# Kernel optimization log

Measured on AMD Instinct MI355X. Metric: run time of the kernel, lower is better.

The kernel has to match this reference:

```python
import jax, jax.numpy as jnp
import numpy as np

N, E = 50000, 800000
IN_CH, HID, OUT_CH = 128, 256, 40
L, R = 3, 16
EPS = 1e-12


def setup_inputs() -> dict:
    key = jax.random.key(0)
    ks = jax.random.split(key, 16)
    s = 0.05
    return {
        'x': jax.random.normal(ks[0], (N, IN_CH), jnp.float32),
        'edge_index': jax.random.randint(ks[1], (2, E), 0, N, dtype=jnp.int64),
        'W_in': jax.random.normal(ks[2], (IN_CH, HID), jnp.float32) * s,
        'b_in': jnp.zeros((HID,), jnp.float32),
        'centers': jax.random.normal(ks[3], (L, R, HID), jnp.float32),
        'log_sigma': jnp.zeros((L, R, HID), jnp.float32),
        'W_rule': jax.random.normal(ks[4], (L, R, HID, HID), jnp.float32) * s,
        'b_rule': jnp.zeros((L, R, HID), jnp.float32),
        'W_self': jax.random.normal(ks[5], (L, HID, HID), jnp.float32) * s,
        'b_self': jnp.zeros((L, HID), jnp.float32),
        'gamma': jnp.ones((L, HID), jnp.float32),
        'beta': jnp.zeros((L, HID), jnp.float32),
        'W_h1': jax.random.normal(ks[6], (HID, HID // 2), jnp.float32) * s,
        'b_h1': jnp.zeros((HID // 2,), jnp.float32),
        'W_h2': jax.random.normal(ks[7], (HID // 2, OUT_CH), jnp.float32) * s,
        'b_h2': jnp.zeros((OUT_CH,), jnp.float32),
    }


def membership(h, c, log_s):
    # Gaussian rule firing, expanded to matmuls to avoid [N,R,H] distance tensor
    inv_s2 = jnp.exp(-2.0 * log_s)                         # [R,H]
    d = (h * h) @ inv_s2.T - 2.0 * (h @ (c * inv_s2).T) \
        + jnp.sum(c * c * inv_s2, axis=-1)                 # [N,R]
    firing = jnp.exp(-0.5 * d)
    return firing / (jnp.sum(firing, axis=-1, keepdims=True) + EPS)


def fmpl(h, src, dst, c, log_s, W_r, b_r, W_s, b_s):
    n = h.shape[0]
    deg = jax.ops.segment_sum(jnp.ones(src.shape[0], h.dtype), dst, num_segments=n)
    agg = jax.ops.segment_sum(h[src], dst, num_segments=n) / jnp.clip(deg, 1.0)[:, None]
    mu = membership(h, c, log_s)                           # [N,R]
    per_rule = jnp.einsum('ni,rio->nro', agg, W_r) + b_r[None]  # [N,R,H]
    fuzzy = jnp.einsum('nr,nro->no', mu, per_rule)
    return h @ W_s + b_s + fuzzy


def batchnorm(x, g, b, eps=1e-5):
    m = jnp.mean(x, axis=0)
    v = jnp.var(x, axis=0)
    return (x - m) * jax.lax.rsqrt(v + eps) * g + b


def reference(x, edge_index, W_in, b_in, centers, log_sigma, W_rule, b_rule,
              W_self, b_self, gamma, beta, W_h1, b_h1, W_h2, b_h2):
    src, dst = edge_index[0], edge_index[1]
    h = jax.nn.relu(x @ W_in + b_in)                       # dropout = identity (eval)
    for l in range(L):
        h_new = fmpl(h, src, dst, centers[l], log_sigma[l], W_rule[l], b_rule[l],
                     W_self[l], b_self[l])
        h_new = jax.nn.relu(batchnorm(h_new, gamma[l], beta[l]))
        h = h + h_new
    logits = jax.nn.relu(h @ W_h1 + b_h1) @ W_h2 + b_h2
    return jax.nn.softmax(logits, axis=-1)
```

## Files before the change

kernel.cpp:

```cpp
#include <hip/hip_runtime.h>
#include <hip/hip_fp16.h>
#include <cstdint>
#include <cstddef>

using u16 = unsigned short;
using u32 = unsigned int;

typedef _Float16 half8 __attribute__((ext_vector_type(8)));
typedef float f32x4 __attribute__((ext_vector_type(4)));

#define MF(a, b, c) __builtin_amdgcn_mfma_f32_16x16x32_f16((a), (b), (c), 0, 0, 0)

static inline int cdiv(int a, int b) { return (a + b - 1) / b; }


__global__ void prep_k(const float* __restrict__ Wr,
                       const float* __restrict__ Ws, const float* __restrict__ br,
                       const float* __restrict__ W_in, const float* __restrict__ W_h1,
                       const float* __restrict__ W_h2,
                       const float* __restrict__ centers, const float* __restrict__ logsig,
                       u16* __restrict__ wcat,
                       u16* __restrict__ winp, u16* __restrict__ wh1p,
                       u16* __restrict__ wh2p,
                       u16* __restrict__ pcB, float* __restrict__ pccc,
                       int* __restrict__ zerobase, int nzero,
                       int Z, int Wb) {
    const int bid = blockIdx.x;
    const int tid = threadIdx.x;
    if (bid < Z) {
        int i = bid * 256 + tid;
        if (i < nzero) zerobase[i] = 0;
        return;
    }
    if (bid < Z + Wb) {
        size_t t = (size_t)(bid - Z) * 256 + tid;
        const size_t PL = 552u * 256u * 8u;
        int l = (int)(t / PL);
        size_t rem = t - (size_t)l * PL;
        int kp = (int)(rem >> 11);
        int o = (int)((rem >> 3) & 255);
        int e = (int)(rem & 7);
        int k = kp * 8 + e;
        float v;
        if (k < 4096)      v = Wr[((((size_t)l * 16 + (k >> 8)) * 256) + (k & 255)) * 256 + o];
        else if (k < 4352) v = Ws[(((size_t)l * 256) + (k - 4096)) * 256 + o];
        else if (k < 4368) v = br[(((size_t)l * 16) + (k - 4352)) * 256 + o];
        else               v = 0.f;
        union { u16 u; _Float16 h; } c; c.h = (_Float16)v;
        wcat[t] = c.u;
        return;
    }
    if (bid < Z + Wb + 128) {
        size_t t = (size_t)(bid - Z - Wb) * 256 + tid;
        int e = (int)(t & 7), o = (int)((t >> 3) & 255);
        int kp = (int)(t >> 11);
        union { u16 u; _Float16 h; } c; c.h = (_Float16)W_in[(size_t)(kp * 8 + e) * 256 + o];
        winp[t] = c.u;
        return;
    }
    if (bid < Z + Wb + 256) {
        size_t t = (size_t)(bid - Z - Wb - 128) * 256 + tid;
        int e = (int)(t & 7), o = (int)((t >> 3) & 127);
        int kp = (int)(t >> 10);
        union { u16 u; _Float16 h; } c; c.h = (_Float16)W_h1[(size_t)(kp * 8 + e) * 128 + o];
        wh1p[t] = c.u;
        return;
    }
    if (bid < Z + Wb + 256 + 24) {
        int t = (bid - Z - Wb - 256) * 256 + tid;
        int e = t & 7, col = (t >> 3) % 48, p = t / 384;
        int k = p * 8 + e;
        float v = (col < 40) ? W_h2[(size_t)k * 40 + col] : 0.f;
        union { u16 u; _Float16 h; } c; c.h = (_Float16)v;
        wh2p[t] = c.u;
        return;
    }
    {
        int lr = bid - (Z + Wb + 256 + 24);
        size_t idx = (size_t)lr * 256 + tid;
        float ls = logsig[idx];
        float inv = expf(-2.f * ls);
        float c = centers[idx];
        union { u16 u; _Float16 h; } c1, c2;
        c1.h = (_Float16)inv;
        c2.h = (_Float16)(-2.f * c * inv);
        pcB[(size_t)lr * 512 + tid] = c1.u;
        pcB[(size_t)lr * 512 + 256 + tid] = c2.u;
        __shared__ float sm[256];
        sm[tid] = c * c * inv;
        __syncthreads();
        for (int s = 128; s > 0; s >>= 1) { if (tid < s) sm[tid] += sm[tid + s]; __syncthreads(); }
        if (tid == 0) pccc[lr] = sm[0];
    }
}


template <int MODE, int NCHUNK>
__launch_bounds__(256, 2)
__global__ void gemm_mn(const u16* __restrict__ A, const u16* __restrict__ A2,
                        const u16* __restrict__ MU, const u16* __restrict__ Bp,
                        const float* __restrict__ bias, const int* __restrict__ bflag,
                        u16* __restrict__ outH, float* __restrict__ bnsum,
                        const u16* __restrict__ pcB, const float* __restrict__ pccc,
                        u16* __restrict__ mu16, int* __restrict__ bflagN,
                        const int* __restrict__ esrc, const int* __restrict__ edst,
                        int* __restrict__ deg, int* __restrict__ indptr,
                        int* __restrict__ cursor, float* __restrict__ deginv,
                        int* __restrict__ ssrc, int* __restrict__ csrctr,
                        int* __restrict__ done, int E, int nrows) {
    __shared__ __align__(16) u16 lds[24576];
    __shared__ float bnbuf[2048];
    __shared__ int ssm[256];
    u16* lA = lds;
    u16* lB = lds + 8192;
    const int tid = threadIdx.x;
    const int row0 = blockIdx.x * 128;
    const int lane = tid & 63;
    const int q = lane >> 4, mm = lane & 15;
    const int wave = tid >> 6;
    int nr = nrows - row0; if (nr > 128) nr = 128;

    if (MODE == 1 && bflag[511] != 0) {
        int bseq = 0;
        auto gbar = [&]() {
            __threadfence();
            __syncthreads();
            ++bseq;
            if (tid == 0) {
                atomicAdd(csrctr, 1);
                while (atomicAdd(csrctr, 0) < (int)gridDim.x * bseq)
                    __builtin_amdgcn_s_sleep(2);
            }
            __syncthreads();
        };
        if (*done == 0) {
            for (int e = blockIdx.x * 256 + tid; e < E; e += (int)gridDim.x * 256)
                atomicAdd(&deg[edst[e]], 1);
            gbar();
            if (blockIdx.x == 0) {
                const int n = nrows;
                const int chunk = (n + 255) >> 8;
                int s0 = tid * chunk, s1 = s0 + chunk;
                if (s1 > n) s1 = n; if (s0 > n) s0 = n;
                int tot = 0;
                for (int i = s0; i < s1; ++i) tot += atomicAdd(&deg[i], 0);
                ssm[tid] = tot; __syncthreads();
                for (int off = 1; off < 256; off <<= 1) {
                    int t = (tid >= off) ? ssm[tid - off] : 0;
                    __syncthreads(); ssm[tid] += t; __syncthreads();
                }
                int base = ssm[tid] - tot;
                for (int i = s0; i < s1; ++i) {
                    int d = atomicAdd(&deg[i], 0);
                    indptr[i] = base; cursor[i] = base;
                    deginv[i] = 1.f / (float)(d > 1 ? d : 1);
                    base += d;
                }
                if (tid == 255) indptr[nrows] = ssm[255];
            }
            gbar();
            for (int e = blockIdx.x * 256 + tid; e < E; e += (int)gridDim.x * 256) {
                int d = edst[e];
                int pos = atomicAdd(&cursor[d], 1);
                ssrc[pos] = esrc[e];
            }
            gbar();
            if (blockIdx.x == 0 && tid == 0) *done = 1;
        }
        if (bflag[blockIdx.x] != 0) {
            for (int node = row0 + wave; node < row0 + 128 && node < nrows; node += 4) {
                int j0 = indptr[node], j1 = indptr[node + 1];
                float a0 = 0, a1 = 0, a2 = 0, a3 = 0;
                for (int j = j0; j < j1; ++j) {
                    int sN = ssrc[j];
                    union { uint2 u; _Float16 h[4]; } hv;
                    hv.u = *(const uint2*)(A2 + (size_t)sN * 256 + lane * 4);
                    a0 += (float)hv.h[0]; a1 += (float)hv.h[1];
                    a2 += (float)hv.h[2]; a3 += (float)hv.h[3];
                }
                float di = deginv[node];
                union { uint2 u; _Float16 h[4]; } o;
                o.h[0] = (_Float16)(a0 * di); o.h[1] = (_Float16)(a1 * di);
                o.h[2] = (_Float16)(a2 * di); o.h[3] = (_Float16)(a3 * di);
                *(uint2*)((u16*)A + (size_t)node * 256 + lane * 4) = o.u;
            }
        }
        __threadfence_block();
        __syncthreads();
    }

    f32x4 acc[2][16];
#pragma unroll
    for (int i = 0; i < 2; ++i)
#pragma unroll
        for (int j = 0; j < 16; ++j) acc[i][j] = (f32x4){0.f, 0.f, 0.f, 0.f};

    int cb = 0, cbEnd = NCHUNK;
    if (MODE == 1 && bflag[blockIdx.x] == 0) { cb = 64; cbEnd = 68; }

    for (; cb < cbEnd; ++cb) {
#pragma unroll
        for (int it = 0; it < 8; ++it) {
            int idx = it * 256 + tid;
            int p = idx >> 8, col = idx & 255;
            uint4 v = *(const uint4*)(Bp + (((size_t)(cb * 8 + p)) * 256 + col) * 8);
            *(uint4*)(lB + (size_t)idx * 8) = v;
        }
#pragma unroll
        for (int it = 0; it < 4; ++it) {
            int idx = it * 256 + tid;
            int p = idx >> 7, row = idx & 127;
            int grow = row0 + row; if (grow >= nrows) grow = nrows - 1;
            uint4 v;
            if (MODE == 0) {
                const float* xr = (const float*)A + (size_t)grow * 128 + cb * 64 + (p << 3);
                float4 f0 = *(const float4*)xr;
                float4 f1 = *(const float4*)(xr + 4);
                union { uint4 u4; _Float16 h[8]; } cv;
                cv.h[0] = (_Float16)f0.x; cv.h[1] = (_Float16)f0.y;
                cv.h[2] = (_Float16)f0.z; cv.h[3] = (_Float16)f0.w;
                cv.h[4] = (_Float16)f1.x; cv.h[5] = (_Float16)f1.y;
                cv.h[6] = (_Float16)f1.z; cv.h[7] = (_Float16)f1.w;
                v = cv.u4;
            } else {
                if (cb < 64) {
                    int r = cb >> 2;
                    int i0 = ((cb & 3) << 6) + (p << 3);
                    v = *(const uint4*)(A + (size_t)grow * 256 + i0);
                    union { u16 u; _Float16 h; } mu; mu.u = MU[(size_t)grow * 16 + r];
                    union { uint4 u4; _Float16 h[8]; } wv; wv.u4 = v;
#pragma unroll
                    for (int j = 0; j < 8; ++j) wv.h[j] = wv.h[j] * mu.h;
                    v = wv.u4;
                } else if (cb < 68) {
                    int i0 = ((cb - 64) << 6) + (p << 3);
                    v = *(const uint4*)(A2 + (size_t)grow * 256 + i0);
                } else {
                    int j0 = p << 3;
                    if (j0 < 16) v = *(const uint4*)(MU + (size_t)grow * 16 + j0);
                    else v = (uint4){0, 0, 0, 0};
                }
            }
            *(uint4*)(lA + (size_t)idx * 8) = v;
        }
        __syncthreads();
#pragma unroll
        for (int kc = 0; kc < 2; ++kc) {
            int pp = kc * 4 + q;
            half8 af0 = *(const half8*)(lA + ((size_t)pp * 128 + wave * 32 + mm) * 8);
            half8 af1 = *(const half8*)(lA + ((size_t)pp * 128 + wave * 32 + 16 + mm) * 8);
#pragma unroll
            for (int nt = 0; nt < 16; ++nt) {
                half8 bf = *(const half8*)(lB + ((size_t)pp * 256 + nt * 16 + mm) * 8);
                acc[0][nt] = MF(af0, bf, acc[0][nt]);
                acc[1][nt] = MF(af1, bf, acc[1][nt]);
            }
        }
        __syncthreads();
    }

    if (MODE == 1) {
#pragma unroll
        for (int nt = 0; nt < 16; ++nt) {
            int cl = nt * 16 + mm;
            float bb = bias[cl];
            float s = 0.f, ss = 0.f;
#pragma unroll
            for (int mt = 0; mt < 2; ++mt) {
#pragma unroll
                for (int r = 0; r < 4; ++r) {
                    int row = wave * 32 + mt * 16 + q * 4 + r;
                    float v = acc[mt][nt][r] + bb;
                    if (row < nr) { s += v; ss += v * v; }
                }
            }
            s += __shfl_xor(s, 16);  s += __shfl_xor(s, 32);
            ss += __shfl_xor(ss, 16); ss += __shfl_xor(ss, 32);
            if (q == 0) {
                bnbuf[(wave * 256 + cl) * 2 + 0] = s;
                bnbuf[(wave * 256 + cl) * 2 + 1] = ss;
            }
        }
        __syncthreads();
        {
            float s  = bnbuf[tid * 2]     + bnbuf[(256 + tid) * 2]
                     + bnbuf[(512 + tid) * 2] + bnbuf[(768 + tid) * 2];
            float ss = bnbuf[tid * 2 + 1] + bnbuf[(256 + tid) * 2 + 1]
                     + bnbuf[(512 + tid) * 2 + 1] + bnbuf[(768 + tid) * 2 + 1];
            atomicAdd(&bnsum[tid], s);
            atomicAdd(&bnsum[256 + tid], ss);
        }
    }

    f32x4 macc0 = (f32x4){0.f, 0.f, 0.f, 0.f};
    f32x4 macc1 = (f32x4){0.f, 0.f, 0.f, 0.f};
#pragma unroll
    for (int h = 0; h < 2; ++h) {
        __syncthreads();
#pragma unroll
        for (int nt = 0; nt < 8; ++nt) {
            int cl = h * 128 + nt * 16 + mm;
            float bb = bias[cl];
#pragma unroll
            for (int mt = 0; mt < 2; ++mt) {
#pragma unroll
                for (int r = 0; r < 4; ++r) {
                    int row = wave * 32 + mt * 16 + q * 4 + r;
                    float v = acc[mt][h * 8 + nt][r] + bb;
                    if (MODE == 0) v = fmaxf(v, 0.f);
                    union { u16 u; _Float16 hh; } cc; cc.hh = (_Float16)v;
                    lds[row * 136 + nt * 16 + mm] = cc.u;
                }
            }
        }
        __syncthreads();
#pragma unroll
        for (int it = 0; it < 8; ++it) {
            int idx = it * 256 + tid;
            int row = idx >> 4, cp = idx & 15;
            if (row < nr) {
                uint4 v = *(const uint4*)(lds + row * 136 + cp * 8);
                *(uint4*)(outH + (size_t)(row0 + row) * 256 + h * 128 + cp * 8) = v;
            }
        }
        if (MODE == 0) {
            const u16* brow = pcB + (size_t)mm * 512;
#pragma unroll
            for (int it2 = 0; it2 < 4; ++it2) {
                int lk = it2 * 32 + q * 8;
                half8 b1 = *(const half8*)(brow + h * 128 + lk);
                half8 b2 = *(const half8*)(brow + 256 + h * 128 + lk);
                half8 a0 = *(const half8*)(lds + ((size_t)(wave * 32 + mm)) * 136 + lk);
                half8 a1 = *(const half8*)(lds + ((size_t)(wave * 32 + 16 + mm)) * 136 + lk);
                macc0 = MF(a0 * a0, b1, macc0);
                macc0 = MF(a0, b2, macc0);
                macc1 = MF(a1 * a1, b1, macc1);
                macc1 = MF(a1, b2, macc1);
            }
        }
    }

    if (MODE == 0) {
        float cc = pccc[mm];
        bool any = false;
#pragma unroll
        for (int g = 0; g < 2; ++g) {
            f32x4 macc = g ? macc1 : macc0;
#pragma unroll
            for (int r = 0; r < 4; ++r) {
                float d = macc[r] + cc;
                float f = expf(-0.5f * d);
                float s = f;
                s += __shfl_xor(s, 1); s += __shfl_xor(s, 2);
                s += __shfl_xor(s, 4); s += __shfl_xor(s, 8);
                int node = row0 + (wave * 2 + g) * 16 + q * 4 + r;
                if (node < nrows) {
                    union { u16 u; _Float16 hh; } c2;
                    c2.hh = (_Float16)(f / (s + 1e-12f));
                    mu16[(size_t)node * 16 + mm] = c2.u;
                    if (c2.u != 0) any = true;
                }
            }
        }
        if (__any(any) && lane == 0) {
            atomicOr(&bflagN[blockIdx.x], 1);
            atomicOr(&bflagN[511], 1);
        }
    }
}


template <int TAIL>
__launch_bounds__(256)
__global__ void upd_k(const u16* __restrict__ pre16, const float* __restrict__ bnsum,
                      const float* __restrict__ gamma, const float* __restrict__ beta,
                      u16* __restrict__ h16,
                      const u16* __restrict__ pcB, const float* __restrict__ pccc,
                      u16* __restrict__ mu16, int* __restrict__ bflag,
                      const u16* __restrict__ wh1p, const float* __restrict__ bh1,
                      const u16* __restrict__ wh2p, const float* __restrict__ bh2,
                      float* __restrict__ outF, int n) {
    const int tid = threadIdx.x;
    __shared__ float l_ab[512];
    __shared__ __align__(16) u16 qt[4][2176];
    {
        float su = bnsum[tid];
        float sq = bnsum[256 + tid];
        float invn = 1.f / (float)n;
        float m = su * invn;
        float al = gamma[tid] * rsqrtf(sq * invn - m * m + 1e-5f);
        l_ab[tid] = al;
        l_ab[256 + tid] = beta[tid] - m * al;
    }
    __syncthreads();

    const int lane = tid & 63, wave = tid >> 6;
    const int q = lane >> 4, mm = lane & 15;
    const int n0 = (blockIdx.x * 4 + wave) * 16;
    if (n0 >= n) return;
    const int node = n0 + mm;
    const bool valid = node < n;
    const int nodeC = valid ? node : n - 1;
    const size_t base = (size_t)nodeC * 256 + q * 8;

    half8 v16[8];
#pragma unroll
    for (int b = 0; b < 8; ++b) {
        int c = b * 32 + q * 8;
        float4 alA = *(const float4*)(l_ab + c);
        float4 alB = *(const float4*)(l_ab + c + 4);
        float4 shA = *(const float4*)(l_ab + 256 + c);
        float4 shB = *(const float4*)(l_ab + 256 + c + 4);
        float aarr[8] = {alA.x, alA.y, alA.z, alA.w, alB.x, alB.y, alB.z, alB.w};
        float harr[8] = {shA.x, shA.y, shA.z, shA.w, shB.x, shB.y, shB.z, shB.w};
        union { uint4 u; _Float16 hh[8]; } p, hv, o;
        p.u  = *(const uint4*)(pre16 + base + b * 32);
        hv.u = *(const uint4*)(h16 + base + b * 32);
#pragma unroll
        for (int j = 0; j < 8; ++j) {
            float v = (float)hv.hh[j] + fmaxf((float)p.hh[j] * aarr[j] + harr[j], 0.f);
            o.hh[j] = (_Float16)v;
        }
        if (TAIL == 1 && valid) *(uint4*)(h16 + base + b * 32) = o.u;
        v16[b] = *(half8*)&o;
    }

    if (TAIL == 1) {
        const u16* brow = pcB + (size_t)mm * 512;
        f32x4 acc = (f32x4){0.f, 0.f, 0.f, 0.f};
#pragma unroll
        for (int it = 0; it < 16; ++it) {
            half8 a = v16[it & 7];
            if (it < 8) a = a * a;
            half8 bb = *(const half8*)(brow + it * 32 + q * 8);
            acc = MF(a, bb, acc);
        }
        float cc = pccc[mm];
        bool any = false;
#pragma unroll
        for (int r = 0; r < 4; ++r) {
            float d = acc[r] + cc;
            float f = expf(-0.5f * d);
            float s = f;
            s += __shfl_xor(s, 1); s += __shfl_xor(s, 2);
            s += __shfl_xor(s, 4); s += __shfl_xor(s, 8);
            int nd = n0 + q * 4 + r;
            if (nd < n) {
                union { u16 u; _Float16 h; } c2;
                c2.h = (_Float16)(f / (s + 1e-12f));
                mu16[(size_t)nd * 16 + mm] = c2.u;
                if (c2.u != 0) any = true;
            }
        }
        if (__any(any) && lane == 0) {
            atomicOr(&bflag[n0 >> 7], 1);
            atomicOr(&bflag[511], 1);
        }
    }

    if (TAIL == 2) {
        u16* qw = qt[wave];
        f32x4 hq[8];
#pragma unroll
        for (int j = 0; j < 8; ++j) hq[j] = (f32x4){0.f, 0.f, 0.f, 0.f};
#pragma unroll
        for (int b = 0; b < 8; ++b) {
            half8 a = v16[b];
            const u16* bp = wh1p + ((size_t)((b * 4 + q) * 128) + mm) * 8;
#pragma unroll
            for (int nt = 0; nt < 8; ++nt) {
                half8 bf = *(const half8*)(bp + nt * 128);
                hq[nt] = MF(a, bf, hq[nt]);
            }
        }
#pragma unroll
        for (int nt = 0; nt < 8; ++nt) {
            int cl = nt * 16 + mm;
            float bb = bh1[cl];
#pragma unroll
            for (int r = 0; r < 4; ++r) {
                float v = fmaxf(hq[nt][r] + bb, 0.f);
                union { u16 u; _Float16 h; } cc; cc.h = (_Float16)v;
                qw[(q * 4 + r) * 136 + cl] = cc.u;
            }
        }
        const bool c2ok = (mm < 8);
        float b0 = bh2[mm], b1 = bh2[16 + mm];
        float b2 = c2ok ? bh2[32 + mm] : 0.f;
        f32x4 hacc[3];
#pragma unroll
        for (int t = 0; t < 3; ++t) hacc[t] = (f32x4){0.f, 0.f, 0.f, 0.f};
#pragma unroll
        for (int c = 0; c < 4; ++c) {
            half8 a = *(const half8*)(qw + (size_t)mm * 136 + c * 32 + q * 8);
#pragma unroll
            for (int t = 0; t < 3; ++t) {
                half8 b = *(const half8*)(wh2p + ((size_t)(c * 4 + q) * 48 + t * 16 + mm) * 8);
                hacc[t] = MF(a, b, hacc[t]);
            }
        }
#pragma unroll
        for (int r = 0; r < 4; ++r) {
            int nd = n0 + q * 4 + r;
            float v0 = hacc[0][r] + b0;
            float v1 = hacc[1][r] + b1;
            float v2 = c2ok ? (hacc[2][r] + b2) : -3e38f;
            float m = fmaxf(fmaxf(v0, v1), v2);
            m = fmaxf(m, __shfl_xor(m, 1)); m = fmaxf(m, __shfl_xor(m, 2));
            m = fmaxf(m, __shfl_xor(m, 4)); m = fmaxf(m, __shfl_xor(m, 8));
            float e0 = expf(v0 - m), e1 = expf(v1 - m);
            float e2 = c2ok ? expf(v2 - m) : 0.f;
            float s = e0 + e1 + e2;
            s += __shfl_xor(s, 1); s += __shfl_xor(s, 2);
            s += __shfl_xor(s, 4); s += __shfl_xor(s, 8);
            float is = 1.f / s;
            if (nd < n) {
                float* op = outF + (size_t)nd * 40;
                op[mm] = e0 * is;
                op[16 + mm] = e1 * is;
                if (c2ok) op[32 + mm] = e2 * is;
            }
        }
    }
}


extern "C" void kernel_launch(void* const* d_in, const int* in_sizes, int n_in,
                              void* d_out, int out_size, void* d_ws, size_t ws_size,
                              hipStream_t stream) {
    const float* x       = (const float*)d_in[0];
    const int*   ei      = (const int*)d_in[1];
    const float* W_in    = (const float*)d_in[2];
    const float* b_in    = (const float*)d_in[3];
    const float* centers = (const float*)d_in[4];
    const float* logsig  = (const float*)d_in[5];
    const float* W_rule  = (const float*)d_in[6];
    const float* b_rule  = (const float*)d_in[7];
    const float* W_self  = (const float*)d_in[8];
    const float* b_self  = (const float*)d_in[9];
    const float* gamma   = (const float*)d_in[10];
    const float* beta    = (const float*)d_in[11];
    const float* W_h1    = (const float*)d_in[12];
    const float* b_h1    = (const float*)d_in[13];
    const float* W_h2    = (const float*)d_in[14];
    const float* b_h2    = (const float*)d_in[15];

    const int N = in_sizes[0] / 128;
    const int E = in_sizes[1] / 2;
    const int* e_src = ei;
    const int* e_dst = ei + E;

    char* w = (char*)d_ws;
    size_t off = 0;
    auto alloc = [&](size_t bytes) -> void* {
        void* p = w + off;
        off = (off + bytes + 255) & ~(size_t)255;
        return p;
    };

    const int gx = cdiv(N, 128);

    u16*   h16    = (u16*)  alloc((size_t)N * 256 * 2);
    u16*   pre16  = (u16*)  alloc((size_t)N * 256 * 2);
    u16*   agg16  = (u16*)  alloc((size_t)N * 256 * 2);
    u16*   mu16   = (u16*)  alloc((size_t)N * 16 * 2);
    u16*   wcat   = (u16*)  alloc((size_t)3 * 552 * 256 * 8 * 2);
    u16*   winp   = (u16*)  alloc((size_t)16 * 256 * 8 * 2);
    u16*   wh1p   = (u16*)  alloc((size_t)32 * 128 * 8 * 2);
    u16*   wh2p   = (u16*)  alloc((size_t)16 * 48 * 8 * 2);
    u16*   pcB    = (u16*)  alloc((size_t)48 * 512 * 2);
    float* pccc   = (float*)alloc((size_t)48 * 4);
    int*   indptr = (int*)  alloc((size_t)(N + 1) * 4);
    int*   cursor = (int*)  alloc((size_t)N * 4);
    float* deginv = (float*)alloc((size_t)N * 4);
    int*   ssrc   = (int*)  alloc((size_t)E * 4);
    const int nzero = N + 3 * 512 + 3 * 512 + 16;
    int*   zerob  = (int*)  alloc((size_t)nzero * 4);
    int*   deg    = zerob;
    int*   bflagA = zerob + N;
    float* bnsumA = (float*)(zerob + N + 3 * 512);
    int*   misc   = zerob + N + 3 * 512 + 3 * 512;
    int*   done   = misc;
    int*   csrctr = misc + 1;

    const int Z = cdiv(nzero, 256);
    const int Wb = 3 * 552 * 256 * 8 / 256;
    const int prep_grid = Z + Wb + 128 + 128 + 24 + 48;

    prep_k<<<prep_grid, 256, 0, stream>>>(W_rule, W_self, b_rule, W_in, W_h1, W_h2,
                                          centers, logsig, wcat, winp, wh1p, wh2p,
                                          pcB, pccc, zerob, nzero, Z, Wb);

    gemm_mn<0, 2><<<gx, 256, 0, stream>>>((const u16*)x, nullptr, nullptr, winp,
                                          b_in, nullptr, h16, nullptr,
                                          pcB, pccc, mu16, bflagA,
                                          nullptr, nullptr, nullptr, nullptr,
                                          nullptr, nullptr, nullptr, nullptr,
                                          nullptr, 0, N);

    for (int l = 0; l < 3; ++l) {
        int* bf = bflagA + l * 512;
        float* bns = bnsumA + l * 512;
        gemm_mn<1, 69><<<gx, 256, 0, stream>>>(agg16, h16, mu16,
                                               wcat + (size_t)l * 552 * 256 * 8,
                                               b_self + l * 256, bf, pre16, bns,
                                               nullptr, nullptr, nullptr, nullptr,
                                               e_src, e_dst, deg, indptr, cursor,
                                               deginv, ssrc, csrctr, done, E, N);
        if (l < 2) {
            upd_k<1><<<cdiv(N, 64), 256, 0, stream>>>(pre16, bns, gamma + l * 256,
                                                      beta + l * 256, h16,
                                                      pcB + (size_t)(l + 1) * 16 * 512,
                                                      pccc + (l + 1) * 16, mu16,
                                                      bflagA + (l + 1) * 512,
                                                      nullptr, nullptr, nullptr, nullptr,
                                                      nullptr, N);
        } else {
            upd_k<2><<<cdiv(N, 64), 256, 0, stream>>>(pre16, bns, gamma + l * 256,
                                                      beta + l * 256, h16,
                                                      nullptr, nullptr, nullptr, nullptr,
                                                      wh1p, b_h1, wh2p, b_h2,
                                                      (float*)d_out, N);
        }
    }
}
```

Measured before the change: 289.2 us.

## Split layer GEMM across two column halves per row block and raise occupancy

The per-layer fused GEMM now launches a 2D grid, with each block computing 128 of the 256 output columns for its 128-row tile. This halves the accumulator registers and the B-tile LDS footprint, so the launch bound can allow four blocks per CU. The grid barrier, the CSR build and the batchnorm partial sums are adjusted to the new block count and column offset. In exchange, both column blocks redo the neighbour aggregation and load the same A tiles, which duplicates gather and memory traffic.

Result: slower. 301.0 us (+4.1%).

```diff
diff --git a/kernel.cpp b/kernel.cpp
--- a/kernel.cpp
+++ b/kernel.cpp
@@ -96,7 +96,7 @@
 
 
 template <int MODE, int NCHUNK>
-__launch_bounds__(256, 2)
+__launch_bounds__(256, MODE == 0 ? 2 : 4)
 __global__ void gemm_mn(const u16* __restrict__ A, const u16* __restrict__ A2,
                         const u16* __restrict__ MU, const u16* __restrict__ Bp,
                         const float* __restrict__ bias, const int* __restrict__ bflag,
@@ -108,19 +108,22 @@
                         int* __restrict__ cursor, float* __restrict__ deginv,
                         int* __restrict__ ssrc, int* __restrict__ csrctr,
                         int* __restrict__ done, int E, int nrows) {
-    __shared__ __align__(16) u16 lds[24576];
-    __shared__ float bnbuf[2048];
+    constexpr int NT = (MODE == 0) ? 16 : 8;
+    constexpr int LDSN = (MODE == 0) ? 24576 : 17408;
+    __shared__ __align__(16) u16 lds[LDSN];
     __shared__ int ssm[256];
     u16* lA = lds;
     u16* lB = lds + 8192;
     const int tid = threadIdx.x;
     const int row0 = blockIdx.x * 128;
+    const int c0 = (MODE == 0) ? 0 : ((int)blockIdx.y * 128);
     const int lane = tid & 63;
     const int q = lane >> 4, mm = lane & 15;
     const int wave = tid >> 6;
     int nr = nrows - row0; if (nr > 128) nr = 128;
 
     if (MODE == 1 && bflag[511] != 0) {
+        const int NB = (int)(gridDim.x * gridDim.y);
         int bseq = 0;
         auto gbar = [&]() {
             __threadfence();
@@ -128,16 +131,16 @@
             ++bseq;
             if (tid == 0) {
                 atomicAdd(csrctr, 1);
-                while (atomicAdd(csrctr, 0) < (int)gridDim.x * bseq)
-                    __builtin_amdgcn_s_sleep(2);
+                while (atomicAdd(csrctr, 0) < NB * bseq) __builtin_amdgcn_s_sleep(2);
             }
             __syncthreads();
         };
+        const int gtid = (int)((blockIdx.y * gridDim.x + blockIdx.x) * 256) + tid;
         if (*done == 0) {
-            for (int e = blockIdx.x * 256 + tid; e < E; e += (int)gridDim.x * 256)
+            for (int e = gtid; e < E; e += NB * 256)
                 atomicAdd(&deg[edst[e]], 1);
             gbar();
-            if (blockIdx.x == 0) {
+            if (blockIdx.x == 0 && blockIdx.y == 0) {
                 const int n = nrows;
                 const int chunk = (n + 255) >> 8;
                 int s0 = tid * chunk, s1 = s0 + chunk;
@@ -159,13 +162,13 @@
                 if (tid == 255) indptr[nrows] = ssm[255];
             }
             gbar();
-            for (int e = blockIdx.x * 256 + tid; e < E; e += (int)gridDim.x * 256) {
+            for (int e = gtid; e < E; e += NB * 256) {
                 int d = edst[e];
                 int pos = atomicAdd(&cursor[d], 1);
                 ssrc[pos] = esrc[e];
             }
             gbar();
-            if (blockIdx.x == 0 && tid == 0) *done = 1;
+            if (blockIdx.x == 0 && blockIdx.y == 0 && tid == 0) *done = 1;
         }
         if (bflag[blockIdx.x] != 0) {
             for (int node = row0 + wave; node < row0 + 128 && node < nrows; node += 4) {
@@ -189,21 +192,21 @@
         __syncthreads();
     }
 
-    f32x4 acc[2][16];
+    f32x4 acc[2][NT];
 #pragma unroll
     for (int i = 0; i < 2; ++i)
 #pragma unroll
-        for (int j = 0; j < 16; ++j) acc[i][j] = (f32x4){0.f, 0.f, 0.f, 0.f};
+        for (int j = 0; j < NT; ++j) acc[i][j] = (f32x4){0.f, 0.f, 0.f, 0.f};
 
     int cb = 0, cbEnd = NCHUNK;
     if (MODE == 1 && bflag[blockIdx.x] == 0) { cb = 64; cbEnd = 68; }
 
     for (; cb < cbEnd; ++cb) {
 #pragma unroll
-        for (int it = 0; it < 8; ++it) {
+        for (int it = 0; it < NT / 2; ++it) {
             int idx = it * 256 + tid;
-            int p = idx >> 8, col = idx & 255;
-            uint4 v = *(const uint4*)(Bp + (((size_t)(cb * 8 + p)) * 256 + col) * 8);
+            int p = idx / (NT * 16), col = idx % (NT * 16);
+            uint4 v = *(const uint4*)(Bp + (((size_t)(cb * 8 + p)) * 256 + c0 + col) * 8);
             *(uint4*)(lB + (size_t)idx * 8) = v;
         }
 #pragma unroll
@@ -250,8 +253,8 @@
             half8 af0 = *(const half8*)(lA + ((size_t)pp * 128 + wave * 32 + mm) * 8);
             half8 af1 = *(const half8*)(lA + ((size_t)pp * 128 + wave * 32 + 16 + mm) * 8);
 #pragma unroll
-            for (int nt = 0; nt < 16; ++nt) {
-                half8 bf = *(const half8*)(lB + ((size_t)pp * 256 + nt * 16 + mm) * 8);
+            for (int nt = 0; nt < NT; ++nt) {
+                half8 bf = *(const half8*)(lB + ((size_t)pp * (NT * 16) + nt * 16 + mm) * 8);
                 acc[0][nt] = MF(af0, bf, acc[0][nt]);
                 acc[1][nt] = MF(af1, bf, acc[1][nt]);
             }
@@ -260,10 +263,11 @@
     }
 
     if (MODE == 1) {
-#pragma unroll
-        for (int nt = 0; nt < 16; ++nt) {
+        float* bnbuf = (float*)lds;
+#pragma unroll
+        for (int nt = 0; nt < NT; ++nt) {
             int cl = nt * 16 + mm;
-            float bb = bias[cl];
+            float bb = bias[c0 + cl];
             float s = 0.f, ss = 0.f;
 #pragma unroll
             for (int mt = 0; mt < 2; ++mt) {
@@ -277,30 +281,31 @@
             s += __shfl_xor(s, 16);  s += __shfl_xor(s, 32);
             ss += __shfl_xor(ss, 16); ss += __shfl_xor(ss, 32);
             if (q == 0) {
-                bnbuf[(wave * 256 + cl) * 2 + 0] = s;
-                bnbuf[(wave * 256 + cl) * 2 + 1] = ss;
+                bnbuf[(wave * 128 + cl) * 2 + 0] = s;
+                bnbuf[(wave * 128 + cl) * 2 + 1] = ss;
             }
         }
         __syncthreads();
         {
-            float s  = bnbuf[tid * 2]     + bnbuf[(256 + tid) * 2]
-                     + bnbuf[(512 + tid) * 2] + bnbuf[(768 + tid) * 2];
-            float ss = bnbuf[tid * 2 + 1] + bnbuf[(256 + tid) * 2 + 1]
-                     + bnbuf[(512 + tid) * 2 + 1] + bnbuf[(768 + tid) * 2 + 1];
-            atomicAdd(&bnsum[tid], s);
-            atomicAdd(&bnsum[256 + tid], ss);
+            int col = tid & 127, part = tid >> 7;
+            float v = bnbuf[(0 * 128 + col) * 2 + part]
+                    + bnbuf[(1 * 128 + col) * 2 + part]
+                    + bnbuf[(2 * 128 + col) * 2 + part]
+                    + bnbuf[(3 * 128 + col) * 2 + part];
+            atomicAdd(&bnsum[part * 256 + c0 + col], v);
         }
     }
 
     f32x4 macc0 = (f32x4){0.f, 0.f, 0.f, 0.f};
     f32x4 macc1 = (f32x4){0.f, 0.f, 0.f, 0.f};
-#pragma unroll
-    for (int h = 0; h < 2; ++h) {
+    constexpr int NH = (MODE == 0) ? 2 : 1;
+#pragma unroll
+    for (int h = 0; h < NH; ++h) {
         __syncthreads();
 #pragma unroll
         for (int nt = 0; nt < 8; ++nt) {
             int cl = h * 128 + nt * 16 + mm;
-            float bb = bias[cl];
+            float bb = bias[c0 + cl];
 #pragma unroll
             for (int mt = 0; mt < 2; ++mt) {
 #pragma unroll
@@ -320,7 +325,8 @@
             int row = idx >> 4, cp = idx & 15;
             if (row < nr) {
                 uint4 v = *(const uint4*)(lds + row * 136 + cp * 8);
-                *(uint4*)(outH + (size_t)(row0 + row) * 256 + h * 128 + cp * 8) = v;
+                *(uint4*)(outH + (size_t)(row0 + row) * 256
+                          + (MODE == 0 ? h * 128 : c0) + cp * 8) = v;
             }
         }
         if (MODE == 0) {
@@ -601,12 +607,12 @@
     for (int l = 0; l < 3; ++l) {
         int* bf = bflagA + l * 512;
         float* bns = bnsumA + l * 512;
-        gemm_mn<1, 69><<<gx, 256, 0, stream>>>(agg16, h16, mu16,
-                                               wcat + (size_t)l * 552 * 256 * 8,
-                                               b_self + l * 256, bf, pre16, bns,
-                                               nullptr, nullptr, nullptr, nullptr,
-                                               e_src, e_dst, deg, indptr, cursor,
-                                               deginv, ssrc, csrctr, done, E, N);
+        gemm_mn<1, 69><<<dim3(gx, 2), 256, 0, stream>>>(agg16, h16, mu16,
+                                                        wcat + (size_t)l * 552 * 256 * 8,
+                                                        b_self + l * 256, bf, pre16, bns,
+                                                        nullptr, nullptr, nullptr, nullptr,
+                                                        e_src, e_dst, deg, indptr, cursor,
+                                                        deginv, ssrc, csrctr, done, E, N);
         if (l < 2) {
             upd_k<1><<<cdiv(N, 64), 256, 0, stream>>>(pre16, bns, gamma + l * 256,
                                                       beta + l * 256, h16,
```
